# Kernel tuning notes

Hardware: AMD Instinct MI355X
Metric: run time of the kernel (lower is better)

Reference implementation:

```python
import jax, jax.numpy as jnp
import numpy as np

N_NODES = 100000
N_EDGES = 3200000
NFEAT, HID, NCLASS = 256, 32, 16


def setup_inputs() -> dict:
    key = jax.random.key(0)
    ks = jax.random.split(key, 6)
    x = jax.random.normal(ks[0], (N_NODES, NFEAT), dtype=jnp.float32)
    edge_index = jax.random.randint(ks[1], (2, N_EDGES), 0, N_NODES, dtype=jnp.int64)
    edge_weight = jax.random.uniform(ks[2], (N_EDGES,), dtype=jnp.float32)
    # Glorot-ish init for the two GCNConv linear weights; bias zeros (PyG default init zeros bias)
    W1 = jax.random.normal(ks[3], (NFEAT, HID), dtype=jnp.float32) * (1.0 / np.sqrt(NFEAT))
    b1 = jnp.zeros((HID,), dtype=jnp.float32)
    W2 = jax.random.normal(ks[4], (HID, NCLASS), dtype=jnp.float32) * (1.0 / np.sqrt(HID))
    b2 = jnp.zeros((NCLASS,), dtype=jnp.float32)
    return {"x": x, "edge_index": edge_index, "edge_weight": edge_weight,
            "W1": W1, "b1": b1, "W2": W2, "b2": b2}


def _gcn_norm(row, col, w, n):
    """PyG gcn_norm: add self-loops (weight 1), symmetric normalization."""
    loop = jnp.arange(n, dtype=row.dtype)
    row = jnp.concatenate([row, loop])
    col = jnp.concatenate([col, loop])
    w = jnp.concatenate([w, jnp.ones((n,), dtype=w.dtype)])
    deg = jax.ops.segment_sum(w, col, num_segments=n)  # degree at target nodes
    dinv = jnp.where(deg > 0, jax.lax.rsqrt(deg), 0.0)
    norm = dinv[row] * w * dinv[col]
    return row, col, norm


def _gcn_conv(x, W, b, row, col, norm, n):
    xw = x @ W                                  # [N, out]
    msg = xw[row] * norm[:, None]               # gather at source + scale
    out = jax.ops.segment_sum(msg, col, num_segments=n)  # scatter-add at target
    return out + b


def reference(x, edge_index, edge_weight, W1, b1, W2, b2):
    n = x.shape[0]
    row, col, norm = _gcn_norm(edge_index[0], edge_index[1], edge_weight, n)
    h = jax.nn.relu(_gcn_conv(x, W1, b1, row, col, norm, n))
    # dropout is identity in eval mode
    logits = _gcn_conv(h, W2, b2, row, col, norm, n)
    return jax.nn.log_softmax(logits, axis=1)
```

## Files before the change

### kernel.cpp

```cpp
#include <hip/hip_runtime.h>

#define N_NODES 100000
#define N_EDGES 3200000
#define NFEAT 256
#define HID 32
#define NCLASS 16

#define NB 64
#define CHUNK (N_EDGES / NB)
#define RN2 32768
#define NR2 ((N_NODES + RN2 - 1) / RN2)
#define BPC 196

#define SCAN_TPB 256
#define SCAN_EPB 1024
#define SCAN_NBLK ((N_NODES + SCAN_EPB - 1) / SCAN_EPB)

#define XPAD 133

__device__ inline unsigned short f2bf(float f) {
    unsigned u = __float_as_uint(f);
    u += 0x7FFFu + ((u >> 16) & 1u);
    return (unsigned short)(u >> 16);
}
__device__ inline float bf2f(unsigned short s) {
    return __uint_as_float((unsigned)s << 16);
}
__device__ inline void bf8_unpack(uint4 g, float* f) {
    f[0] = __uint_as_float(g.x << 16); f[1] = __uint_as_float(g.x & 0xFFFF0000u);
    f[2] = __uint_as_float(g.y << 16); f[3] = __uint_as_float(g.y & 0xFFFF0000u);
    f[4] = __uint_as_float(g.z << 16); f[5] = __uint_as_float(g.z & 0xFFFF0000u);
    f[6] = __uint_as_float(g.w << 16); f[7] = __uint_as_float(g.w & 0xFFFF0000u);
}

__global__ __launch_bounds__(1024) void k_count(const int* __restrict__ col,
                                                unsigned* __restrict__ H,
                                                unsigned short* __restrict__ pos) {
    __shared__ unsigned hist[RN2 / 2];
    int t = threadIdx.x, b = blockIdx.x, r = blockIdx.y;
    int base = r * RN2;
    const int* cc = col + (size_t)b * CHUNK;
    unsigned short* pp = pos + (size_t)b * CHUNK;
    for (int i = t; i < RN2 / 2; i += 1024) hist[i] = 0;
    __syncthreads();
    for (int i = t; i < CHUNK; i += 1024) {
        unsigned d = (unsigned)cc[i] - (unsigned)base;
        if (d < RN2) {
            unsigned old = atomicAdd(&hist[d >> 1], 1u << ((d & 1) * 16));
            pp[i] = (unsigned short)((old >> ((d & 1) * 16)) & 0xFFFFu);
        }
    }
    __syncthreads();
    int lim = min(RN2, N_NODES - base);
    unsigned* Hb = H + (size_t)b * N_NODES;
    for (int i = t; i < lim; i += 1024)
        Hb[base + i] = (hist[i >> 1] >> ((i & 1) * 16)) & 0xFFFFu;
}

__global__ void k_prefix16(const unsigned* __restrict__ H,
                           unsigned short* __restrict__ SP, int* __restrict__ cnt) {
    int n = blockIdx.x * 256 + threadIdx.x;
    if (n >= N_NODES) return;
    unsigned run = 0;
    #pragma unroll 8
    for (int b = 0; b < NB; ++b) {
        size_t i = (size_t)b * N_NODES + n;
        unsigned v = H[i];
        SP[i] = (unsigned short)run;
        run += v;
    }
    cnt[n] = (int)run;
}

__global__ __launch_bounds__(SCAN_TPB) void k_scanA(const int* __restrict__ cnt,
                                                    int* __restrict__ offs,
                                                    int* __restrict__ bsum) {
    __shared__ int s[SCAN_TPB];
    int t = threadIdx.x;
    int base = blockIdx.x * SCAN_EPB + t * 4;
    int v0 = (base + 0 < N_NODES) ? cnt[base + 0] : 0;
    int v1 = (base + 1 < N_NODES) ? cnt[base + 1] : 0;
    int v2 = (base + 2 < N_NODES) ? cnt[base + 2] : 0;
    int v3 = (base + 3 < N_NODES) ? cnt[base + 3] : 0;
    int sum = v0 + v1 + v2 + v3;
    s[t] = sum;
    __syncthreads();
    for (int off = 1; off < SCAN_TPB; off <<= 1) {
        int x = (t >= off) ? s[t - off] : 0;
        __syncthreads();
        s[t] += x;
        __syncthreads();
    }
    int excl = s[t] - sum;
    if (t == SCAN_TPB - 1) bsum[blockIdx.x] = s[t];
    int run = excl;
    if (base + 0 < N_NODES) offs[base + 0] = run; run += v0;
    if (base + 1 < N_NODES) offs[base + 1] = run; run += v1;
    if (base + 2 < N_NODES) offs[base + 2] = run; run += v2;
    if (base + 3 < N_NODES) offs[base + 3] = run;
}

__global__ __launch_bounds__(128) void k_scanB(int* __restrict__ bsum) {
    __shared__ int s[128];
    int t = threadIdx.x;
    int v = (t < SCAN_NBLK) ? bsum[t] : 0;
    s[t] = v;
    __syncthreads();
    for (int off = 1; off < 128; off <<= 1) {
        int x = (t >= off) ? s[t - off] : 0;
        __syncthreads();
        s[t] += x;
        __syncthreads();
    }
    if (t < SCAN_NBLK) bsum[t] = s[t] - v;
}

__global__ __launch_bounds__(SCAN_TPB) void k_scanC(int* __restrict__ offs,
                                                    const int* __restrict__ bsum) {
    int t = threadIdx.x;
    int add = bsum[blockIdx.x];
    int base = blockIdx.x * SCAN_EPB + t * 4;
    #pragma unroll
    for (int i = 0; i < 4; ++i) {
        int idx = base + i;
        if (idx < N_NODES) offs[idx] += add;
    }
    if (blockIdx.x == 0 && t == 0) offs[N_NODES] = N_EDGES;
}

__global__ __launch_bounds__(256) void k_emit(const int* __restrict__ row,
                                              const int* __restrict__ col,
                                              const float* __restrict__ w,
                                              const int* __restrict__ offs,
                                              const unsigned short* __restrict__ SP,
                                              const unsigned short* __restrict__ pos,
                                              float2* __restrict__ ein) {
    int bid = blockIdx.x;
    int xcd = bid & 7;
    int q = bid >> 3;
    int m = q / BPC;
    int j = q - m * BPC;
    int b = xcd + 8 * m;
    int i0 = j * 256 + threadIdx.x;
    if (i0 >= CHUNK) return;
    size_t e = (size_t)b * CHUNK + i0;
    int c = col[e];
    unsigned p = (unsigned)offs[c] + (unsigned)SP[(size_t)b * N_NODES + c]
               + (unsigned)pos[e];
    ein[p] = make_float2(__int_as_float(row[e]), w[e]);
}

__global__ void k_deg(const float2* __restrict__ ein, const int* __restrict__ offs,
                      float* __restrict__ dinv) {
    int idx = blockIdx.x * 256 + threadIdx.x;
    int n = idx >> 2, l = idx & 3;
    if (n >= N_NODES) return;
    int s = offs[n], e = offs[n + 1];
    float sum = 0.f;
    for (int p = s + l; p < e; p += 4) sum += ein[p].y;
    sum += __shfl_xor(sum, 1, 4);
    sum += __shfl_xor(sum, 2, 4);
    if (l == 0) dinv[n] = rsqrtf(1.0f + sum);
}

__global__ __launch_bounds__(256) void k_gemm1s(const float* __restrict__ x,
                                                const float* __restrict__ W1,
                                                unsigned short* __restrict__ xwp) {
    __shared__ float sWc[32 * HID];
    __shared__ float sX[32 * XPAD];
    int t = threadIdx.x;
    long rowbase = (long)blockIdx.x * 128;
    int kbase = blockIdx.y * 128;
    unsigned short* xw = xwp + (size_t)blockIdx.y * N_NODES * HID;
    int tr = t >> 3;
    int tc = t & 7;
    float acc[4][4] = {};
    for (int k0 = kbase; k0 < kbase + 128; k0 += 32) {
        *(float4*)&sWc[t * 4] = *(const float4*)&W1[k0 * HID + t * 4];
        #pragma unroll
        for (int p = 0; p < 4; ++p) {
            int rt = (t >> 3) + p * 32;
            int kk = (t & 7) * 4;
            long grow = rowbase + rt;
            float4 v = make_float4(0.f, 0.f, 0.f, 0.f);
            if (grow < N_NODES) v = *(const float4*)&x[grow * NFEAT + k0 + kk];
            sX[(kk + 0) * XPAD + rt] = v.x; sX[(kk + 1) * XPAD + rt] = v.y;
            sX[(kk + 2) * XPAD + rt] = v.z; sX[(kk + 3) * XPAD + rt] = v.w;
        }
        __syncthreads();
        #pragma unroll 8
        for (int kk = 0; kk < 32; ++kk) {
            float xv[4], wv[4];
            xv[0] = sX[kk * XPAD + tr * 4 + 0];
            xv[1] = sX[kk * XPAD + tr * 4 + 1];
            xv[2] = sX[kk * XPAD + tr * 4 + 2];
            xv[3] = sX[kk * XPAD + tr * 4 + 3];
            *(float4*)&wv[0] = *(float4*)&sWc[kk * HID + tc * 4];
            #pragma unroll
            for (int m = 0; m < 4; ++m)
                #pragma unroll
                for (int n = 0; n < 4; ++n)
                    acc[m][n] = fmaf(xv[m], wv[n], acc[m][n]);
        }
        __syncthreads();
    }
    #pragma unroll
    for (int m = 0; m < 4; ++m) {
        long r = rowbase + tr * 4 + m;
        if (r < N_NODES) {
            ushort4 o;
            o.x = f2bf(acc[m][0]); o.y = f2bf(acc[m][1]);
            o.z = f2bf(acc[m][2]); o.w = f2bf(acc[m][3]);
            *(ushort4*)&xw[r * HID + tc * 4] = o;
        }
    }
}

__global__ void k_comb(const unsigned short* __restrict__ xwp,
                       ushort4* __restrict__ xwb) {
    int i = blockIdx.x * 256 + threadIdx.x;
    const ushort4* p0 = (const ushort4*)xwp;
    const ushort4* p1 = p0 + 800000;
    ushort4 a = p0[i], b = p1[i];
    ushort4 o;
    o.x = f2bf(bf2f(a.x) + bf2f(b.x));
    o.y = f2bf(bf2f(a.y) + bf2f(b.y));
    o.z = f2bf(bf2f(a.z) + bf2f(b.z));
    o.w = f2bf(bf2f(a.w) + bf2f(b.w));
    xwb[i] = o;
}

__global__ __launch_bounds__(256) void k_gather1(const unsigned short* __restrict__ xwb,
                                                 const float* __restrict__ dinv,
                                                 const float2* __restrict__ ein,
                                                 const int* __restrict__ offs,
                                                 const float* __restrict__ b1,
                                                 float* __restrict__ h) {
    int idx = blockIdx.x * 256 + threadIdx.x;
    int n = idx >> 3, l = idx & 7;
    int c4 = l * 4;
    const ushort4* xb = (const ushort4*)xwb;
    float di = dinv[n];
    ushort4 q = xb[(long)n * 8 + l];
    float4 acc = make_float4(bf2f(q.x) * di, bf2f(q.y) * di,
                             bf2f(q.z) * di, bf2f(q.w) * di);
    int s = offs[n], e = offs[n + 1];
    for (int p0 = s; p0 < e; p0 += 8) {
        int pl = p0 + l;
        float2 pr = (pl < e) ? ein[pl] : make_float2(__int_as_float(n), 0.f);
        int ri = __float_as_int(pr.x);
        pr.y *= dinv[ri];
        #pragma unroll
        for (int j = 0; j < 8; ++j) {
            int r = __shfl(ri, j, 8);
            float nm = __shfl(pr.y, j, 8);
            ushort4 g = xb[(long)r * 8 + l];
            acc.x = fmaf(bf2f(g.x), nm, acc.x);
            acc.y = fmaf(bf2f(g.y), nm, acc.y);
            acc.z = fmaf(bf2f(g.z), nm, acc.z);
            acc.w = fmaf(bf2f(g.w), nm, acc.w);
        }
    }
    float4 bb = *(const float4*)&b1[c4];
    acc.x = fmaxf(fmaf(acc.x, di, bb.x), 0.f);
    acc.y = fmaxf(fmaf(acc.y, di, bb.y), 0.f);
    acc.z = fmaxf(fmaf(acc.z, di, bb.z), 0.f);
    acc.w = fmaxf(fmaf(acc.w, di, bb.w), 0.f);
    *(float4*)&h[(long)n * HID + c4] = acc;
}

__global__ __launch_bounds__(256) void k_gemm2(const float* __restrict__ h,
                                               const float* __restrict__ W2,
                                               unsigned short* __restrict__ hwb) {
    __shared__ float sH[64][33];
    __shared__ float sW2[HID * NCLASS];
    int t = threadIdx.x;
    if (t < 128) {
        int idx = t * 4;
        *(float4*)&sW2[idx] = *(const float4*)&W2[idx];
    }
    long base = (long)blockIdx.x * 64;
    #pragma unroll
    for (int i = 0; i < 2; ++i) {
        int idx = t + i * 256;
        int rt = idx >> 3, kk = (idx & 7) * 4;
        long gr = base + rt;
        float4 v = make_float4(0.f, 0.f, 0.f, 0.f);
        if (gr < N_NODES) v = *(const float4*)&h[gr * HID + kk];
        sH[rt][kk + 0] = v.x; sH[rt][kk + 1] = v.y;
        sH[rt][kk + 2] = v.z; sH[rt][kk + 3] = v.w;
    }
    __syncthreads();
    int r = t >> 2, c4 = (t & 3) * 4;
    float acc[4] = {};
    #pragma unroll
    for (int k = 0; k < HID; ++k) {
        float hv = sH[r][k];
        float wv[4];
        *(float4*)&wv[0] = *(float4*)&sW2[k * NCLASS + c4];
        #pragma unroll
        for (int n = 0; n < 4; ++n) acc[n] = fmaf(hv, wv[n], acc[n]);
    }
    long gr = base + r;
    if (gr < N_NODES) {
        ushort4 o;
        o.x = f2bf(acc[0]); o.y = f2bf(acc[1]);
        o.z = f2bf(acc[2]); o.w = f2bf(acc[3]);
        *(ushort4*)&hwb[gr * NCLASS + c4] = o;
    }
}

__global__ __launch_bounds__(256) void k_gather2(const unsigned short* __restrict__ hwb,
                                                 const float* __restrict__ dinv,
                                                 const float2* __restrict__ ein,
                                                 const int* __restrict__ offs,
                                                 const float* __restrict__ b2,
                                                 float* __restrict__ out) {
    int idx = blockIdx.x * 256 + threadIdx.x;
    int n = idx >> 1, l = idx & 1;
    if (n >= N_NODES) return;
    int c8 = l * 8;
    const uint4* hb = (const uint4*)hwb;
    float di = dinv[n];
    float acc[8], f[8];
    bf8_unpack(hb[(long)n * 2 + l], f);
    #pragma unroll
    for (int k = 0; k < 8; ++k) acc[k] = f[k] * di;
    int s = offs[n], e = offs[n + 1];
    for (int p0 = s; p0 < e; p0 += 8) {
        float2 pr[4];
        int rr[4];
        #pragma unroll
        for (int k = 0; k < 4; ++k) {
            int pl = p0 + k * 2 + l;
            pr[k] = (pl < e) ? ein[pl] : make_float2(__int_as_float(n), 0.f);
            rr[k] = __float_as_int(pr[k].x);
            pr[k].y *= dinv[rr[k]];
        }
        #pragma unroll
        for (int k = 0; k < 4; ++k) {
            #pragma unroll
            for (int j = 0; j < 2; ++j) {
                int r = __shfl(rr[k], j, 2);
                float nm = __shfl(pr[k].y, j, 2);
                bf8_unpack(hb[(long)r * 2 + l], f);
                #pragma unroll
                for (int q = 0; q < 8; ++q) acc[q] = fmaf(f[q], nm, acc[q]);
            }
        }
    }
    float4 bb0 = *(const float4*)&b2[c8];
    float4 bb1 = *(const float4*)&b2[c8 + 4];
    float v[8];
    v[0] = fmaf(acc[0], di, bb0.x); v[1] = fmaf(acc[1], di, bb0.y);
    v[2] = fmaf(acc[2], di, bb0.z); v[3] = fmaf(acc[3], di, bb0.w);
    v[4] = fmaf(acc[4], di, bb1.x); v[5] = fmaf(acc[5], di, bb1.y);
    v[6] = fmaf(acc[6], di, bb1.z); v[7] = fmaf(acc[7], di, bb1.w);
    float m = v[0];
    #pragma unroll
    for (int k = 1; k < 8; ++k) m = fmaxf(m, v[k]);
    m = fmaxf(m, __shfl_xor(m, 1, 2));
    float sum = 0.f;
    #pragma unroll
    for (int k = 0; k < 8; ++k) sum += __expf(v[k] - m);
    sum += __shfl_xor(sum, 1, 2);
    float ls = m + __logf(sum);
    float4 o0 = make_float4(v[0] - ls, v[1] - ls, v[2] - ls, v[3] - ls);
    float4 o1 = make_float4(v[4] - ls, v[5] - ls, v[6] - ls, v[7] - ls);
    *(float4*)&out[(long)n * NCLASS + c8] = o0;
    *(float4*)&out[(long)n * NCLASS + c8 + 4] = o1;
}

extern "C" void kernel_launch(void* const* d_in, const int* in_sizes, int n_in,
                              void* d_out, int out_size, void* d_ws, size_t ws_size,
                              hipStream_t stream) {
    const float* x  = (const float*)d_in[0];
    const int*   ei = (const int*)d_in[1];
    const float* w  = (const float*)d_in[2];
    const float* W1 = (const float*)d_in[3];
    const float* b1 = (const float*)d_in[4];
    const float* W2 = (const float*)d_in[5];
    const float* b2 = (const float*)d_in[6];
    float* out = (float*)d_out;

    const int* row = ei;
    const int* col = ei + N_EDGES;

    float* ws = (float*)d_ws;
    float2* ein = (float2*)ws;
    unsigned* H = (unsigned*)(ws + 2 * (size_t)N_EDGES);
    unsigned short* pos = (unsigned short*)(ws + 2 * (size_t)N_EDGES + (size_t)NB * N_NODES);
    float* h = (float*)pos;
    float* dinv = ws + 2 * (size_t)N_EDGES + (size_t)NB * N_NODES + N_EDGES;
    int* cnt = (int*)(dinv + N_NODES);
    int* offs = cnt + N_NODES;
    int* bsum = offs + N_NODES + 1;
    size_t xwp_off = (size_t)(2 * (size_t)N_EDGES + (size_t)NB * N_NODES + N_EDGES
                              + 3 * N_NODES + 1 + 128);
    xwp_off = (xwp_off + 3) & ~(size_t)3;
    unsigned short* xwp = (unsigned short*)(ws + xwp_off);
    unsigned short* xwb = (unsigned short*)(ws + xwp_off + 3200000);
    unsigned short* hwb = xwb + (size_t)N_NODES * HID;
    unsigned short* SP = hwb + (size_t)N_NODES * NCLASS;

    const int B = 256;

    k_count<<<dim3(NB, NR2), 1024, 0, stream>>>(col, H, pos);
    k_prefix16<<<(N_NODES + B - 1) / B, B, 0, stream>>>(H, SP, cnt);
    k_scanA<<<SCAN_NBLK, SCAN_TPB, 0, stream>>>(cnt, offs, bsum);
    k_scanB<<<1, 128, 0, stream>>>(bsum);
    k_scanC<<<SCAN_NBLK, SCAN_TPB, 0, stream>>>(offs, bsum);
    k_emit<<<8 * 8 * BPC, B, 0, stream>>>(row, col, w, offs, SP, pos, ein);

    k_deg<<<(N_NODES * 4 + B - 1) / B, B, 0, stream>>>(ein, offs, dinv);

    k_gemm1s<<<dim3((N_NODES + 127) / 128, 2), 256, 0, stream>>>(x, W1, xwp);
    k_comb<<<(N_NODES * HID / 4) / B, B, 0, stream>>>(xwp, (ushort4*)xwb);
    k_gather1<<<(N_NODES * 8) / B, B, 0, stream>>>(xwb, dinv, ein, offs, b1, h);

    k_gemm2<<<(N_NODES + 63) / 64, B, 0, stream>>>(h, W2, hwb);
    k_gather2<<<(N_NODES * 2 + B - 1) / B, B, 0, stream>>>(hwb, dinv, ein, offs, b2, out);
}
```

Before: 263.5 us.

## Replace single-pass edge emit with two-level bucketed scatter by target octant

The direct scatter of edges into CSR order is replaced by a two-pass scheme. Edges are first partitioned by target-node octant per sub-chunk, using per-block counts and a global scan to compute bucket bases. Each bucket is then scattered into its final CSR position, so that writes and SP/offs lookups stay within a narrower address range and gain locality. This adds two extra kernels and an extra pass that writes and reads an intermediate edge buffer, reusing workspace regions.

```diff
diff --git a/kernel.cpp b/kernel.cpp
--- a/kernel.cpp
+++ b/kernel.cpp
@@ -10,7 +10,9 @@
 #define CHUNK (N_EDGES / NB)
 #define RN2 32768
 #define NR2 ((N_NODES + RN2 - 1) / RN2)
-#define BPC 196
+#define OCT 12500
+#define SUBC 12500
+#define NREG 2048
 
 #define SCAN_TPB 256
 #define SCAN_EPB 1024
@@ -128,26 +130,87 @@
     if (blockIdx.x == 0 && t == 0) offs[N_NODES] = N_EDGES;
 }
 
-__global__ __launch_bounds__(256) void k_emit(const int* __restrict__ row,
-                                              const int* __restrict__ col,
-                                              const float* __restrict__ w,
-                                              const int* __restrict__ offs,
-                                              const unsigned short* __restrict__ SP,
-                                              const unsigned short* __restrict__ pos,
-                                              float2* __restrict__ ein) {
+__global__ __launch_bounds__(256) void k_ac2(const int* __restrict__ col,
+                                             unsigned* __restrict__ AC2) {
+    __shared__ unsigned c8[8];
+    int t = threadIdx.x, b = blockIdx.x >> 2, s = blockIdx.x & 3;
+    if (t < 8) c8[t] = 0;
+    __syncthreads();
+    const int* cc = col + (size_t)b * CHUNK + (size_t)s * SUBC;
+    for (int i = t; i < SUBC; i += 256) {
+        int o = cc[i] / OCT;
+        atomicAdd(&c8[o], 1u);
+    }
+    __syncthreads();
+    if (t < 8) AC2[(size_t)blockIdx.x * 8 + t] = c8[t];
+}
+
+__global__ __launch_bounds__(256) void k_acscan(const unsigned* __restrict__ AC2,
+                                                unsigned* __restrict__ bases) {
+    __shared__ unsigned s[256];
+    int t = threadIdx.x;
+    unsigned v[8], sum = 0;
+    #pragma unroll
+    for (int k = 0; k < 8; ++k) { v[k] = AC2[t * 8 + k]; sum += v[k]; }
+    s[t] = sum;
+    __syncthreads();
+    for (int off = 1; off < 256; off <<= 1) {
+        unsigned x = (t >= off) ? s[t - off] : 0;
+        __syncthreads();
+        s[t] += x;
+        __syncthreads();
+    }
+    unsigned run = s[t] - sum;
+    #pragma unroll
+    for (int k = 0; k < 8; ++k) { bases[t * 8 + k] = run; run += v[k]; }
+    if (t == 255) bases[NREG] = run;
+}
+
+__global__ __launch_bounds__(256) void k_bucketA(const int* __restrict__ row,
+                                                 const int* __restrict__ col,
+                                                 const float* __restrict__ w,
+                                                 const unsigned short* __restrict__ pos,
+                                                 const unsigned* __restrict__ bases,
+                                                 unsigned long long* __restrict__ ABsw,
+                                                 unsigned* __restrict__ ABc) {
+    __shared__ unsigned cur[8];
+    int t = threadIdx.x, b = blockIdx.x >> 2, s = blockIdx.x & 3;
+    int g0 = blockIdx.x * 8;
+    if (t < 8) cur[t] = bases[g0 + t];
+    __syncthreads();
+    size_t eb = (size_t)b * CHUNK + (size_t)s * SUBC;
+    for (int i = t; i < SUBC; i += 256) {
+        size_t e = eb + i;
+        int c = col[e];
+        int o = c / OCT;
+        unsigned slot = atomicAdd(&cur[o], 1u);
+        ABsw[slot] = ((unsigned long long)__float_as_uint(w[e]) << 32) | (unsigned)row[e];
+        ABc[slot] = (unsigned)c | ((unsigned)pos[e] << 17);
+    }
+}
+
+__global__ __launch_bounds__(256) void k_bucketB(const unsigned long long* __restrict__ ABsw,
+                                                 const unsigned* __restrict__ ABc,
+                                                 const int* __restrict__ offs,
+                                                 const unsigned short* __restrict__ SP,
+                                                 const unsigned* __restrict__ bases,
+                                                 float2* __restrict__ ein) {
     int bid = blockIdx.x;
-    int xcd = bid & 7;
-    int q = bid >> 3;
-    int m = q / BPC;
-    int j = q - m * BPC;
-    int b = xcd + 8 * m;
-    int i0 = j * 256 + threadIdx.x;
-    if (i0 >= CHUNK) return;
-    size_t e = (size_t)b * CHUNK + i0;
-    int c = col[e];
-    unsigned p = (unsigned)offs[c] + (unsigned)SP[(size_t)b * N_NODES + c]
-               + (unsigned)pos[e];
-    ein[p] = make_float2(__int_as_float(row[e]), w[e]);
+    int o = bid & 7;
+    int idx = bid >> 3;
+    int b = idx >> 2;
+    int g = idx * 8 + o;
+    unsigned start = bases[g], end = bases[g + 1];
+    const unsigned short* SPb = SP + (size_t)b * N_NODES;
+    for (unsigned i = start + threadIdx.x; i < end; i += 256) {
+        unsigned long long sw = __builtin_nontemporal_load(&ABsw[i]);
+        unsigned cp = __builtin_nontemporal_load(&ABc[i]);
+        int c = cp & 0x1FFFF;
+        unsigned pp = cp >> 17;
+        unsigned p = (unsigned)offs[c] + (unsigned)SPb[c] + pp;
+        ein[p] = make_float2(__uint_as_float((unsigned)sw),
+                             __uint_as_float((unsigned)(sw >> 32)));
+    }
 }
 
 __global__ void k_deg(const float2* __restrict__ ein, const int* __restrict__ offs,
@@ -389,6 +452,7 @@
     float* ws = (float*)d_ws;
     float2* ein = (float2*)ws;
     unsigned* H = (unsigned*)(ws + 2 * (size_t)N_EDGES);
+    unsigned long long* ABsw = (unsigned long long*)H;
     unsigned short* pos = (unsigned short*)(ws + 2 * (size_t)N_EDGES + (size_t)NB * N_NODES);
     float* h = (float*)pos;
     float* dinv = ws + 2 * (size_t)N_EDGES + (size_t)NB * N_NODES + N_EDGES;
@@ -399,9 +463,12 @@
                               + 3 * N_NODES + 1 + 128);
     xwp_off = (xwp_off + 3) & ~(size_t)3;
     unsigned short* xwp = (unsigned short*)(ws + xwp_off);
+    unsigned* ABc = (unsigned*)xwp;
     unsigned short* xwb = (unsigned short*)(ws + xwp_off + 3200000);
     unsigned short* hwb = xwb + (size_t)N_NODES * HID;
     unsigned short* SP = hwb + (size_t)N_NODES * NCLASS;
+    unsigned* AC2 = (unsigned*)(SP + (size_t)NB * N_NODES);
+    unsigned* bases = AC2 + NREG;
 
     const int B = 256;
 
@@ -410,7 +477,11 @@
     k_scanA<<<SCAN_NBLK, SCAN_TPB, 0, stream>>>(cnt, offs, bsum);
     k_scanB<<<1, 128, 0, stream>>>(bsum);
     k_scanC<<<SCAN_NBLK, SCAN_TPB, 0, stream>>>(offs, bsum);
-    k_emit<<<8 * 8 * BPC, B, 0, stream>>>(row, col, w, offs, SP, pos, ein);
+
+    k_ac2<<<NB * 4, B, 0, stream>>>(col, AC2);
+    k_acscan<<<1, B, 0, stream>>>(AC2, bases);
+    k_bucketA<<<NB * 4, B, 0, stream>>>(row, col, w, pos, bases, ABsw, ABc);
+    k_bucketB<<<NREG, B, 0, stream>>>(ABsw, ABc, offs, SP, bases, ein);
 
     k_deg<<<(N_NODES * 4 + B - 1) / B, B, 0, stream>>>(ein, offs, dinv);
 
```

Measured after the change: 348.0 us. 1.32x slower.
